# Optimization experiments

Hardware: AMD Instinct MI355X
Metric: run time of the kernel (lower is better)

## Reference

```python
import jax, jax.numpy as jnp
import numpy as np


def setup_inputs() -> dict:
    key = jax.random.key(0)
    ks = jax.random.split(key, 7)
    B, N, H, BIN = 16, 96, 256, 11
    std = 0.1
    return {
        "inputs": jax.random.normal(ks[0], (B, N, H), dtype=jnp.float32),
        "bin_features": jax.random.normal(ks[1], (B, N, N, BIN), dtype=jnp.float32),
        "W_atom": jax.random.normal(ks[2], (H, H), dtype=jnp.float32) * std,
        "W_bin": jax.random.normal(ks[3], (BIN, H), dtype=jnp.float32) * std,
        "b_bin": jnp.zeros((H,), dtype=jnp.float32),
        "w_score": jax.random.normal(ks[4], (H, 1), dtype=jnp.float32) * std,
        "b_score": jnp.zeros((1,), dtype=jnp.float32),
    }


def reference(inputs, bin_features, W_atom, W_bin, b_bin, w_score, b_score):
    # inputs: [B, N, H]; bin_features: [B, N, N, BIN]
    h1 = inputs[:, None, :, :]            # [B, 1, N, H] (atom_hiddens1)
    h2 = inputs[:, :, None, :]            # [B, N, 1, H] (atom_hiddens2)
    atom_pair = h1 + h2                   # [B, N, N, H]
    # Dense(no bias) on pair + Dense(bias) on bin features, then relu
    att_hidden = jax.nn.relu(
        jnp.einsum("bijh,hk->bijk", atom_pair, W_atom)
        + jnp.einsum("bijc,ck->bijk", bin_features, W_bin)
        + b_bin
    )                                      # [B, N, N, H]
    att_score = jax.nn.sigmoid(jnp.einsum("bijk,ko->bijo", att_hidden, w_score) + b_score)  # [B, N, N, 1]
    # att_context = score * atom_hiddens1 (broadcast over i), summed over j (axis 2)
    context = jnp.einsum("bijo,bjh->bih", att_score, inputs)  # [B, N, H]
    return context, atom_pair
```

## Files before the change

kernel.cpp:

```cpp
#include <hip/hip_runtime.h>
#include <math.h>

#define BB 16
#define NN 96
#define HH 256
#define NBIN 11
#define NBPAD 12
#define IB 2

template <int CTRL>
__device__ __forceinline__ float dpp_add(float x) {
    int t = __builtin_amdgcn_update_dpp(0, __float_as_int(x),
                                        CTRL, 0xf, 0xf, true);
    return x + __int_as_float(t);
}

__device__ __forceinline__ float wave64_sum_uniform(float x) {
    x = dpp_add<0x111>(x);
    x = dpp_add<0x112>(x);
    x = dpp_add<0x114>(x);
    x = dpp_add<0x118>(x);
    x = dpp_add<0x142>(x);
    x = dpp_add<0x143>(x);
    return __int_as_float(__builtin_amdgcn_readlane(__float_as_int(x), 63));
}

#define ROWS_PER_BLOCK 3

__global__ __launch_bounds__(HH) void proj_kernel(
    const float* __restrict__ inputs,
    const float* __restrict__ W_atom,
    const float* __restrict__ b_bin,
    float* __restrict__ proj)
{
    __shared__ float rows[ROWS_PER_BLOCK][HH];
    const int r0 = blockIdx.x * ROWS_PER_BLOCK;
    const int k  = threadIdx.x;

    #pragma unroll
    for (int r = 0; r < ROWS_PER_BLOCK; ++r)
        rows[r][k] = inputs[(size_t)(r0 + r) * HH + k];
    __syncthreads();

    float acc[ROWS_PER_BLOCK];
    #pragma unroll
    for (int r = 0; r < ROWS_PER_BLOCK; ++r) acc[r] = 0.f;

    #pragma unroll 8
    for (int h = 0; h < HH; ++h) {
        const float w = W_atom[(size_t)h * HH + k];
        #pragma unroll
        for (int r = 0; r < ROWS_PER_BLOCK; ++r)
            acc[r] = fmaf(rows[r][h], w, acc[r]);
    }

    const float halfb = 0.5f * b_bin[k];
    #pragma unroll
    for (int r = 0; r < ROWS_PER_BLOCK; ++r)
        proj[(size_t)(r0 + r) * HH + k] = acc[r] + halfb;
}

__global__ __launch_bounds__(256, 4) void pair_ctx_kernel(
    const float* __restrict__ inputs,
    const float* __restrict__ bin_features,
    const float* __restrict__ W_bin,
    const float* __restrict__ w_score,
    const float* __restrict__ b_score,
    const float* __restrict__ proj,
    float* __restrict__ atom_pair,
    float* __restrict__ context)
{
    const int blk  = blockIdx.x;
    const int b    = blk / (NN / IB);
    const int ip   = blk % (NN / IB);
    const int bi0  = b * NN + IB * ip;
    const int lane = threadIdx.x & 63;
    const int wave = threadIdx.x >> 6;
    const int k4   = lane << 2;

    __shared__ float binf[IB * NN * NBPAD];
    __shared__ float partial[3][IB * HH];

    {
        const float* bp = bin_features + (size_t)bi0 * NN * NBIN;
        for (int t = threadIdx.x; t < IB * NN * NBIN; t += 256)
            binf[(t / NBIN) * NBPAD + (t % NBIN)] = bp[t];
    }

    const float4 in_i0 = *(const float4*)(inputs + (size_t)bi0 * HH + k4);
    const float4 in_i1 = *(const float4*)(inputs + (size_t)(bi0 + 1) * HH + k4);
    const float4 pr_i0 = *(const float4*)(proj   + (size_t)bi0 * HH + k4);
    const float4 pr_i1 = *(const float4*)(proj   + (size_t)(bi0 + 1) * HH + k4);
    const float4 ws    = *(const float4*)(w_score + k4);
    const float  bsc   = b_score[0];

    float4 wb[NBIN];
    #pragma unroll
    for (int c = 0; c < NBIN; ++c)
        wb[c] = *(const float4*)(W_bin + c * HH + k4);

    const float* inb  = inputs + (size_t)b * NN * HH + k4;
    const float* prb  = proj   + (size_t)b * NN * HH + k4;
    float*       apb0 = atom_pair + (size_t)bi0 * NN * HH + k4;
    float*       apb1 = atom_pair + (size_t)(bi0 + 1) * NN * HH + k4;

    __syncthreads();

    float4 acc0 = make_float4(0.f, 0.f, 0.f, 0.f);
    float4 acc1 = make_float4(0.f, 0.f, 0.f, 0.f);

    for (int t = 0; t < 12; ++t) {
        const int j0 = wave + 8 * t;

        float4 inj[2], prj[2];
        #pragma unroll
        for (int u = 0; u < 2; ++u) {
            inj[u] = *(const float4*)(inb + (size_t)(j0 + 4 * u) * HH);
            prj[u] = *(const float4*)(prb + (size_t)(j0 + 4 * u) * HH);
        }

        #pragma unroll
        for (int u = 0; u < 2; ++u) {
            float4 ap;
            ap.x = in_i0.x + inj[u].x;  ap.y = in_i0.y + inj[u].y;
            ap.z = in_i0.z + inj[u].z;  ap.w = in_i0.w + inj[u].w;
            *(float4*)(apb0 + (size_t)(j0 + 4 * u) * HH) = ap;
            ap.x = in_i1.x + inj[u].x;  ap.y = in_i1.y + inj[u].y;
            ap.z = in_i1.z + inj[u].z;  ap.w = in_i1.w + inj[u].w;
            *(float4*)(apb1 + (size_t)(j0 + 4 * u) * HH) = ap;
        }

        float part[4];
        #pragma unroll
        for (int u = 0; u < 2; ++u) {
            const int j = j0 + 4 * u;
            #pragma unroll
            for (int ii = 0; ii < 2; ++ii) {
                const float4* bf4 =
                    (const float4*)&binf[(ii * NN + j) * NBPAD];
                const float4 bq0 = bf4[0];
                const float4 bq1 = bf4[1];
                const float4 bq2 = bf4[2];
                const float bc[NBIN] = { bq0.x, bq0.y, bq0.z, bq0.w,
                                         bq1.x, bq1.y, bq1.z, bq1.w,
                                         bq2.x, bq2.y, bq2.z };

                const float4 pri = ii ? pr_i1 : pr_i0;
                float4 v;
                v.x = pri.x + prj[u].x;  v.y = pri.y + prj[u].y;
                v.z = pri.z + prj[u].z;  v.w = pri.w + prj[u].w;
                #pragma unroll
                for (int c = 0; c < NBIN; ++c) {
                    v.x = fmaf(bc[c], wb[c].x, v.x);
                    v.y = fmaf(bc[c], wb[c].y, v.y);
                    v.z = fmaf(bc[c], wb[c].z, v.z);
                    v.w = fmaf(bc[c], wb[c].w, v.w);
                }
                v.x = fmaxf(v.x, 0.f); v.y = fmaxf(v.y, 0.f);
                v.z = fmaxf(v.z, 0.f); v.w = fmaxf(v.w, 0.f);
                part[2 * u + ii] =
                    v.x * ws.x + v.y * ws.y + v.z * ws.z + v.w * ws.w;
            }
        }

        float s[4];
        #pragma unroll
        for (int p = 0; p < 4; ++p) {
            const float tot = wave64_sum_uniform(part[p]);
            s[p] = 1.f / (1.f + __expf(-(tot + bsc)));
        }

        #pragma unroll
        for (int u = 0; u < 2; ++u) {
            acc0.x = fmaf(s[2 * u],     inj[u].x, acc0.x);
            acc0.y = fmaf(s[2 * u],     inj[u].y, acc0.y);
            acc0.z = fmaf(s[2 * u],     inj[u].z, acc0.z);
            acc0.w = fmaf(s[2 * u],     inj[u].w, acc0.w);
            acc1.x = fmaf(s[2 * u + 1], inj[u].x, acc1.x);
            acc1.y = fmaf(s[2 * u + 1], inj[u].y, acc1.y);
            acc1.z = fmaf(s[2 * u + 1], inj[u].z, acc1.z);
            acc1.w = fmaf(s[2 * u + 1], inj[u].w, acc1.w);
        }
    }

    if (wave > 0) {
        *(float4*)(&partial[wave - 1][k4]) = acc0;
        *(float4*)(&partial[wave - 1][HH + k4]) = acc1;
    }
    __syncthreads();
    if (wave == 0) {
        #pragma unroll
        for (int w = 0; w < 3; ++w) {
            const float4 p0 = *(const float4*)(&partial[w][k4]);
            const float4 p1 = *(const float4*)(&partial[w][HH + k4]);
            acc0.x += p0.x; acc0.y += p0.y; acc0.z += p0.z; acc0.w += p0.w;
            acc1.x += p1.x; acc1.y += p1.y; acc1.z += p1.z; acc1.w += p1.w;
        }
        *(float4*)(context + (size_t)bi0 * HH + k4) = acc0;
        *(float4*)(context + (size_t)(bi0 + 1) * HH + k4) = acc1;
    }
}

extern "C" void kernel_launch(void* const* d_in, const int* in_sizes, int n_in,
                              void* d_out, int out_size, void* d_ws, size_t ws_size,
                              hipStream_t stream)
{
    const float* inputs       = (const float*)d_in[0];
    const float* bin_features = (const float*)d_in[1];
    const float* W_atom       = (const float*)d_in[2];
    const float* W_bin        = (const float*)d_in[3];
    const float* b_bin        = (const float*)d_in[4];
    const float* w_score      = (const float*)d_in[5];
    const float* b_score      = (const float*)d_in[6];

    float* context   = (float*)d_out;
    float* atom_pair = (float*)d_out + (size_t)BB * NN * HH;

    float* proj = (float*)d_ws;

    proj_kernel<<<(BB * NN) / ROWS_PER_BLOCK, HH, 0, stream>>>(
        inputs, W_atom, b_bin, proj);

    pair_ctx_kernel<<<(BB * NN) / IB, 256, 0, stream>>>(
        inputs, bin_features, W_bin, w_score, b_score, proj,
        atom_pair, context);
}
```

Measured before the change: 50.37 us.

## Split atom_pair writes into separate block roles from score/context compute

Triples the grid so each group of three blocks has two blocks that only stream atom_pair rows (one row i each) and one block that computes attention scores and context. The compute block no longer issues the large atom_pair stores, so the store-bound and ALU-bound work can overlap across different blocks. It also drops the occupancy hint from launch bounds and replaces the sigmoid division with a hardware reciprocal. The cost is extra blocks that each reread the inputs rows, plus a slightly less precise reciprocal.

```diff
diff --git a/kernel.cpp b/kernel.cpp
--- a/kernel.cpp
+++ b/kernel.cpp
@@ -60,7 +60,7 @@
         proj[(size_t)(r0 + r) * HH + k] = acc[r] + halfb;
 }
 
-__global__ __launch_bounds__(256, 4) void pair_ctx_kernel(
+__global__ __launch_bounds__(256) void pair_ctx_kernel(
     const float* __restrict__ inputs,
     const float* __restrict__ bin_features,
     const float* __restrict__ W_bin,
@@ -70,13 +70,38 @@
     float* __restrict__ atom_pair,
     float* __restrict__ context)
 {
-    const int blk  = blockIdx.x;
-    const int b    = blk / (NN / IB);
-    const int ip   = blk % (NN / IB);
-    const int bi0  = b * NN + IB * ip;
+    const int g    = blockIdx.x / 3;
+    const int role = blockIdx.x % 3;
     const int lane = threadIdx.x & 63;
     const int wave = threadIdx.x >> 6;
     const int k4   = lane << 2;
+
+    if (role < 2) {
+        const int bi = 2 * g + role;
+        const int b  = bi / NN;
+        const float4 in_i = *(const float4*)(inputs + (size_t)bi * HH + k4);
+        const float* inb  = inputs + (size_t)b * NN * HH + k4;
+        float*       apb  = atom_pair + (size_t)bi * NN * HH + k4;
+
+        for (int t = 0; t < 6; ++t) {
+            const int j0 = wave + 16 * t;
+            float4 r4[4];
+            #pragma unroll
+            for (int u = 0; u < 4; ++u)
+                r4[u] = *(const float4*)(inb + (size_t)(j0 + 4 * u) * HH);
+            #pragma unroll
+            for (int u = 0; u < 4; ++u) {
+                float4 ap;
+                ap.x = in_i.x + r4[u].x;  ap.y = in_i.y + r4[u].y;
+                ap.z = in_i.z + r4[u].z;  ap.w = in_i.w + r4[u].w;
+                *(float4*)(apb + (size_t)(j0 + 4 * u) * HH) = ap;
+            }
+        }
+        return;
+    }
+
+    const int bi0 = 2 * g;
+    const int b   = bi0 / NN;
 
     __shared__ float binf[IB * NN * NBPAD];
     __shared__ float partial[3][IB * HH];
@@ -87,10 +112,8 @@
             binf[(t / NBIN) * NBPAD + (t % NBIN)] = bp[t];
     }
 
-    const float4 in_i0 = *(const float4*)(inputs + (size_t)bi0 * HH + k4);
-    const float4 in_i1 = *(const float4*)(inputs + (size_t)(bi0 + 1) * HH + k4);
-    const float4 pr_i0 = *(const float4*)(proj   + (size_t)bi0 * HH + k4);
-    const float4 pr_i1 = *(const float4*)(proj   + (size_t)(bi0 + 1) * HH + k4);
+    const float4 pr_i0 = *(const float4*)(proj + (size_t)bi0 * HH + k4);
+    const float4 pr_i1 = *(const float4*)(proj + (size_t)(bi0 + 1) * HH + k4);
     const float4 ws    = *(const float4*)(w_score + k4);
     const float  bsc   = b_score[0];
 
@@ -99,10 +122,8 @@
     for (int c = 0; c < NBIN; ++c)
         wb[c] = *(const float4*)(W_bin + c * HH + k4);
 
-    const float* inb  = inputs + (size_t)b * NN * HH + k4;
-    const float* prb  = proj   + (size_t)b * NN * HH + k4;
-    float*       apb0 = atom_pair + (size_t)bi0 * NN * HH + k4;
-    float*       apb1 = atom_pair + (size_t)(bi0 + 1) * NN * HH + k4;
+    const float* inb = inputs + (size_t)b * NN * HH + k4;
+    const float* prb = proj   + (size_t)b * NN * HH + k4;
 
     __syncthreads();
 
@@ -117,17 +138,6 @@
         for (int u = 0; u < 2; ++u) {
             inj[u] = *(const float4*)(inb + (size_t)(j0 + 4 * u) * HH);
             prj[u] = *(const float4*)(prb + (size_t)(j0 + 4 * u) * HH);
-        }
-
-        #pragma unroll
-        for (int u = 0; u < 2; ++u) {
-            float4 ap;
-            ap.x = in_i0.x + inj[u].x;  ap.y = in_i0.y + inj[u].y;
-            ap.z = in_i0.z + inj[u].z;  ap.w = in_i0.w + inj[u].w;
-            *(float4*)(apb0 + (size_t)(j0 + 4 * u) * HH) = ap;
-            ap.x = in_i1.x + inj[u].x;  ap.y = in_i1.y + inj[u].y;
-            ap.z = in_i1.z + inj[u].z;  ap.w = in_i1.w + inj[u].w;
-            *(float4*)(apb1 + (size_t)(j0 + 4 * u) * HH) = ap;
         }
 
         float part[4];
@@ -167,7 +177,7 @@
         #pragma unroll
         for (int p = 0; p < 4; ++p) {
             const float tot = wave64_sum_uniform(part[p]);
-            s[p] = 1.f / (1.f + __expf(-(tot + bsc)));
+            s[p] = __builtin_amdgcn_rcpf(1.f + __expf(-(tot + bsc)));
         }
 
         #pragma unroll
@@ -221,7 +231,7 @@
     proj_kernel<<<(BB * NN) / ROWS_PER_BLOCK, HH, 0, stream>>>(
         inputs, W_atom, b_bin, proj);
 
-    pair_ctx_kernel<<<(BB * NN) / IB, 256, 0, stream>>>(
+    pair_ctx_kernel<<<(BB * NN / 2) * 3, 256, 0, stream>>>(
         inputs, bin_features, W_bin, w_score, b_score, proj,
         atom_pair, context);
 }
```

Result: slower. 61.79 us (+22.7%).
